# Kernel tuning notes

Measured on AMD Instinct MI355X. Metric: run time of the kernel, lower is better.

The kernel has to match this reference:

```python
import jax, jax.numpy as jnp
import numpy as np

B, T, N, D = 16, 12, 2048, 128  # T*D == 12*hidden_dim, D == hidden_dim (structural constraint)


def _lin(key, out_dim, in_dim):
    k1, k2 = jax.random.split(key)
    s = 1.0 / np.sqrt(in_dim)
    W = jax.random.uniform(k1, (out_dim, in_dim), jnp.float32, -s, s)
    b = jax.random.uniform(k2, (out_dim,), jnp.float32, -s, s)
    return W, b


def setup_inputs() -> dict:
    key = jax.random.key(0)
    ks = jax.random.split(key, 12)
    x = jax.random.normal(ks[0], (B, T, N, D), jnp.float32)
    Wd1, bd1 = _lin(ks[1], D, 12 * D)      # conv_down[0] (1x1 conv == linear over channels)
    Wd2, bd2 = _lin(ks[2], D, D)           # conv_down[3]
    Wq, bq = _lin(ks[3], D, D)
    Wk, bk = _lin(ks[4], D, D)
    Wv, bv = _lin(ks[5], D, D)
    Wu1, bu1 = _lin(ks[6], 12 * D, D)      # conv_up[0]
    Wu2, bu2 = _lin(ks[7], 12 * D, 12 * D) # conv_up[3]
    gamma = jnp.ones((D,), jnp.float32)
    beta = jnp.zeros((D,), jnp.float32)
    Wr1, br1 = _lin(ks[8], D, D)
    Wr2, br2 = _lin(ks[9], D, D)
    Wi1, bi1 = _lin(ks[10], D, D)
    Wi2, bi2 = _lin(ks[11], D, D)
    return dict(x=x, Wd1=Wd1, bd1=bd1, Wd2=Wd2, bd2=bd2, Wq=Wq, bq=bq, Wk=Wk, bk=bk,
                Wv=Wv, bv=bv, Wu1=Wu1, bu1=bu1, Wu2=Wu2, bu2=bu2, gamma=gamma, beta=beta,
                Wr1=Wr1, br1=br1, Wr2=Wr2, br2=br2, Wi1=Wi1, bi1=bi1, Wi2=Wi2, bi2=bi2)


def _mlp(x, W1, b1, W2, b2):
    # Linear -> GELU(exact, torch default) -> (Dropout=identity in eval) -> Linear
    return jax.nn.gelu(x @ W1.T + b1, approximate=False) @ W2.T + b2


def reference(x, Wd1, bd1, Wd2, bd2, Wq, bq, Wk, bk, Wv, bv, Wu1, bu1, Wu2, bu2,
              gamma, beta, Wr1, br1, Wr2, br2, Wi1, bi1, Wi2, bi2):
    Bx, Tx, Nx, d = x.shape
    # ---- node self-attention branch ----
    xt = jnp.transpose(x, (0, 2, 1, 3)).reshape(Bx, Nx, Tx * d)        # [B,N,T*d]
    y = jax.nn.relu(xt @ Wd1.T + bd1) @ Wd2.T + bd2                     # conv_down: [B,N,d]
    q = y @ Wq.T + bq
    k = y @ Wk.T + bk
    v = y @ Wv.T + bv
    scale = 1.0 / jnp.sqrt(jnp.float32(d // 2))                         # dk = hidden_dim // 2
    scores = jax.nn.softmax(jnp.einsum('bnd,bmd->bnm', q, k) * scale, axis=-1)
    o = jnp.einsum('bnm,bmd->bnd', scores, v)                           # [B,N,d]
    o = jax.nn.relu(o @ Wu1.T + bu1) @ Wu2.T + bu2                      # conv_up: [B,N,12d]
    out_node = jnp.transpose(o.reshape(Bx, Nx, Tx, d), (0, 2, 1, 3))    # [B,T,N,d]
    # ---- residual + LayerNorm ----
    h1 = out_node + x
    mu = jnp.mean(h1, axis=-1, keepdims=True)
    var = jnp.mean(jnp.square(h1 - mu), axis=-1, keepdims=True)
    hn = (h1 - mu) / jnp.sqrt(var + 1e-5) * gamma + beta
    # ---- FFT dual-path MLP over time axis ----
    hf = jnp.fft.rfft(hn, axis=1)                                        # [B,T//2+1,N,d] complex
    re, im = jnp.real(hf), jnp.imag(hf)
    hr = _mlp(re, Wr1, br1, Wr2, br2) - _mlp(im, Wi1, bi1, Wi2, bi2)
    hi = _mlp(re, Wi1, bi1, Wi2, bi2) + _mlp(im, Wr1, br1, Wr2, br2)
    hc = jax.lax.complex(hr, hi)
    out = jnp.fft.irfft(hc, n=Tx, axis=1) + x
    return out
```

## Files before the change

### kernel.cpp

```cpp
#include <hip/hip_runtime.h>
#include <math.h>

#define T_ 12
#define N_ 2048
#define D_ 128
#define ND_ 262144
#define TND_ 3145728L

typedef __attribute__((ext_vector_type(8))) short short8;
typedef __attribute__((ext_vector_type(4))) float f32x4;

__device__ __forceinline__ ushort f2b(float f) {
  unsigned u = __float_as_uint(f);
  u += 0x7fffu + ((u >> 16) & 1u);
  return (ushort)(u >> 16);
}
__device__ __forceinline__ float b2f(ushort s) {
  return __uint_as_float(((unsigned)s) << 16);
}

__device__ __forceinline__ void gload16(const ushort* g, ushort* lds) {
  __builtin_amdgcn_global_load_lds(
      (const __attribute__((address_space(1))) void*)g,
      (__attribute__((address_space(3))) void*)lds, 16, 0, 0);
}

__constant__ float COS12[12] = {
    1.0f, 0.8660254037844387f, 0.5f, 0.0f, -0.5f, -0.8660254037844387f,
    -1.0f, -0.8660254037844387f, -0.5f, 0.0f, 0.5f, 0.8660254037844387f};
__constant__ float SIN12[12] = {
    0.0f, 0.5f, 0.8660254037844387f, 1.0f, 0.8660254037844387f, 0.5f,
    0.0f, -0.5f, -0.8660254037844387f, -1.0f, -0.8660254037844387f, -0.5f};

template <int ACT, int OUT>
__global__ __launch_bounds__(256) void mgemm(
    const ushort* __restrict__ A, const ushort* __restrict__ B,
    const float* __restrict__ bias, void* __restrict__ Cv,
    int K, int lda, int ldb, int ldc, float alpha,
    long sAb, long sBb, long sCb, int off0, int off1) {
  __shared__ ushort As[4096];
  __shared__ ushort Bs[4096];
  const int tid = threadIdx.x;
  const int w = tid >> 6;
  const int l = tid & 63;
  const int lr = l & 15;
  const int lg = l >> 4;
  const int row0 = blockIdx.y * 128;
  const int col0 = blockIdx.x * 128;
  const ushort* Ap = A + sAb * blockIdx.z;
  const ushort* Bp = B + sBb * blockIdx.z;

  f32x4 acc[2][8];
#pragma unroll
  for (int i = 0; i < 2; ++i)
#pragma unroll
    for (int j = 0; j < 8; ++j) acc[i][j] = (f32x4){0.f, 0.f, 0.f, 0.f};

  const int ba = w, bb2 = w + 4;
  const ushort* Apl = Ap + (long)(row0 + ba * 16 + lr) * lda + lg * 8;
  const ushort* Apl2 = Ap + (long)(row0 + bb2 * 16 + lr) * lda + lg * 8;
  const ushort* Bpl = Bp + (long)(col0 + ba * 16 + lr) * ldb + lg * 8;
  const ushort* Bpl2 = Bp + (long)(col0 + bb2 * 16 + lr) * ldb + lg * 8;
  for (int k0 = 0; k0 < K; k0 += 32) {
    gload16(Apl + k0, As + ba * 512);
    gload16(Apl2 + k0, As + bb2 * 512);
    gload16(Bpl + k0, Bs + ba * 512);
    gload16(Bpl2 + k0, Bs + bb2 * 512);
    __syncthreads();
    const short8 a0 = *(const short8*)(As + (w * 2 + 0) * 512 + l * 8);
    const short8 a1 = *(const short8*)(As + (w * 2 + 1) * 512 + l * 8);
#pragma unroll
    for (int ni = 0; ni < 8; ++ni) {
      const short8 bfr = *(const short8*)(Bs + ni * 512 + l * 8);
      acc[0][ni] = __builtin_amdgcn_mfma_f32_16x16x32_bf16(a0, bfr, acc[0][ni], 0, 0, 0);
      acc[1][ni] = __builtin_amdgcn_mfma_f32_16x16x32_bf16(a1, bfr, acc[1][ni], 0, 0, 0);
    }
    __syncthreads();
  }

  const long Cz = sCb * blockIdx.z;
#pragma unroll
  for (int mi = 0; mi < 2; ++mi) {
    const int grow0 = row0 + w * 32 + mi * 16 + lg * 4;
    if (OUT == 2) {
      ushort* C = (ushort*)Cv;
#pragma unroll
      for (int ni = 0; ni < 8; ++ni) {
        const int c = col0 + ni * 16 + lr;
        const float bv = bias ? bias[c] : 0.f;
        ushort4 pk;
        float v0 = acc[mi][ni][0] * alpha + bv;
        float v1 = acc[mi][ni][1] * alpha + bv;
        float v2 = acc[mi][ni][2] * alpha + bv;
        float v3 = acc[mi][ni][3] * alpha + bv;
        if (ACT == 1) { v0 = fmaxf(v0, 0.f); v1 = fmaxf(v1, 0.f); v2 = fmaxf(v2, 0.f); v3 = fmaxf(v3, 0.f); }
        pk.x = f2b(v0); pk.y = f2b(v1); pk.z = f2b(v2); pk.w = f2b(v3);
        *(ushort4*)(C + (long)c * ldc + grow0) = pk;
      }
    } else {
#pragma unroll
      for (int ni = 0; ni < 8; ++ni) {
        const int c = col0 + ni * 16 + lr;
        const float bv = bias ? bias[c] : 0.f;
        const int cm = c + (c < 128 ? off0 : off1);
#pragma unroll
        for (int r = 0; r < 4; ++r) {
          float v = acc[mi][ni][r] * alpha + bv;
          if (ACT == 1) v = fmaxf(v, 0.f);
          if (ACT == 2) v = 0.5f * v * (1.0f + erff(v * 0.7071067811865475f));
          const long off = Cz + (long)(grow0 + r) * ldc + cm;
          if (OUT == 0) ((float*)Cv)[off] = v;
          else ((ushort*)Cv)[off] = f2b(v);
        }
      }
    }
  }
}

__global__ __launch_bounds__(256) void mgemm_ln(
    const ushort* __restrict__ A, const ushort* __restrict__ B,
    const float* __restrict__ bias, const float* __restrict__ x,
    const float* __restrict__ gamma, const float* __restrict__ beta,
    float* __restrict__ hn) {
  const int K = 1536;
  __shared__ ushort As[4096];
  __shared__ ushort Bs[4096];
  const int tid = threadIdx.x;
  const int w = tid >> 6;
  const int l = tid & 63;
  const int lr = l & 15;
  const int lg = l >> 4;
  const int row0 = blockIdx.y * 128;
  const int t = blockIdx.x;
  const int col0 = t * 128;

  f32x4 acc[2][8];
#pragma unroll
  for (int i = 0; i < 2; ++i)
#pragma unroll
    for (int j = 0; j < 8; ++j) acc[i][j] = (f32x4){0.f, 0.f, 0.f, 0.f};

  const int ba = w, bb2 = w + 4;
  const ushort* Apl = A + (long)(row0 + ba * 16 + lr) * K + lg * 8;
  const ushort* Apl2 = A + (long)(row0 + bb2 * 16 + lr) * K + lg * 8;
  const ushort* Bpl = B + (long)(col0 + ba * 16 + lr) * K + lg * 8;
  const ushort* Bpl2 = B + (long)(col0 + bb2 * 16 + lr) * K + lg * 8;
  for (int k0 = 0; k0 < K; k0 += 32) {
    gload16(Apl + k0, As + ba * 512);
    gload16(Apl2 + k0, As + bb2 * 512);
    gload16(Bpl + k0, Bs + ba * 512);
    gload16(Bpl2 + k0, Bs + bb2 * 512);
    __syncthreads();
    const short8 a0 = *(const short8*)(As + (w * 2 + 0) * 512 + l * 8);
    const short8 a1 = *(const short8*)(As + (w * 2 + 1) * 512 + l * 8);
#pragma unroll
    for (int ni = 0; ni < 8; ++ni) {
      const short8 bfr = *(const short8*)(Bs + ni * 512 + l * 8);
      acc[0][ni] = __builtin_amdgcn_mfma_f32_16x16x32_bf16(a0, bfr, acc[0][ni], 0, 0, 0);
      acc[1][ni] = __builtin_amdgcn_mfma_f32_16x16x32_bf16(a1, bfr, acc[1][ni], 0, 0, 0);
    }
    __syncthreads();
  }

#pragma unroll
  for (int mi = 0; mi < 2; ++mi) {
#pragma unroll
    for (int r = 0; r < 4; ++r) {
      const int gr = row0 + w * 32 + mi * 16 + lg * 4 + r;
      const int bb = gr >> 11;
      const int nn = gr & 2047;
      const long base = ((long)(bb * 12 + t) << 18) + (long)nn * 128;
      float h[8];
      float s1 = 0.f, s2 = 0.f;
#pragma unroll
      for (int ni = 0; ni < 8; ++ni) {
        const int d = ni * 16 + lr;
        const float v = acc[mi][ni][r] + bias[col0 + d] + x[base + d];
        h[ni] = v;
        s1 += v;
        s2 += v * v;
      }
#pragma unroll
      for (int m = 1; m < 16; m <<= 1) {
        s1 += __shfl_xor(s1, m);
        s2 += __shfl_xor(s2, m);
      }
      const float mu = s1 * (1.f / 128.f);
      const float rstd = rsqrtf(s2 * (1.f / 128.f) - mu * mu + 1e-5f);
#pragma unroll
      for (int ni = 0; ni < 8; ++ni) {
        const int d = ni * 16 + lr;
        hn[base + d] = (h[ni] - mu) * rstd * gamma[d] + beta[d];
      }
    }
  }
}

__global__ __launch_bounds__(256) void softmax_k(const float* __restrict__ S,
                                                 ushort* __restrict__ P) {
  const long row = ((long)blockIdx.y * N_ + blockIdx.x) * N_;
  const float* p = S + row;
  const int tid = threadIdx.x;
  float v[8];
  float mx = -3.4e38f;
#pragma unroll
  for (int j = 0; j < 8; ++j) {
    v[j] = p[tid + 256 * j];
    mx = fmaxf(mx, v[j]);
  }
  __shared__ float red[256];
  red[tid] = mx;
  __syncthreads();
  for (int s = 128; s > 0; s >>= 1) {
    if (tid < s) red[tid] = fmaxf(red[tid], red[tid + s]);
    __syncthreads();
  }
  mx = red[0];
  __syncthreads();
  float sum = 0.0f;
#pragma unroll
  for (int j = 0; j < 8; ++j) {
    v[j] = expf(v[j] - mx);
    sum += v[j];
  }
  red[tid] = sum;
  __syncthreads();
  for (int s = 128; s > 0; s >>= 1) {
    if (tid < s) red[tid] += red[tid + s];
    __syncthreads();
  }
  const float inv = 1.0f / red[0];
#pragma unroll
  for (int j = 0; j < 8; ++j) P[row + tid + 256 * j] = f2b(v[j] * inv);
}

__global__ __launch_bounds__(256) void rfft_k(const float* __restrict__ hn,
                                              ushort* __restrict__ re,
                                              ushort* __restrict__ im) {
  const long i = (long)blockIdx.x * 256 + threadIdx.x;
  const int bb = (int)(i >> 18);
  const int nd = (int)(i & (ND_ - 1));
  float ht[12];
#pragma unroll
  for (int t = 0; t < 12; ++t) ht[t] = hn[((long)(bb * T_ + t) << 18) + nd];
#pragma unroll
  for (int f = 0; f < 7; ++f) {
    float sr = 0.0f, si = 0.0f;
#pragma unroll
    for (int t = 0; t < 12; ++t) {
      const int k = (f * t) % 12;
      sr = fmaf(ht[t], COS12[k], sr);
      si = fmaf(ht[t], SIN12[k], si);
    }
    const long off = ((long)(bb * 7 + f) << 18) + nd;
    re[off] = f2b(sr);
    im[off] = f2b(-si);
  }
}

__global__ __launch_bounds__(256) void irfft_k(const float* __restrict__ hr,
                                               const float* __restrict__ hi,
                                               const float* __restrict__ x,
                                               float* __restrict__ out) {
  const long i = (long)blockIdx.x * 256 + threadIdx.x;
  const int bb = (int)(i >> 18);
  const int nd = (int)(i & (ND_ - 1));
  float r[7], m[7];
#pragma unroll
  for (int f = 0; f < 7; ++f) {
    const long off = ((long)(bb * 7 + f) << 18) + nd;
    r[f] = hr[off];
    m[f] = hi[off];
  }
#pragma unroll
  for (int t = 0; t < 12; ++t) {
    float s = r[0] + ((t & 1) ? -r[6] : r[6]);
#pragma unroll
    for (int f = 1; f < 6; ++f) {
      const int k = (f * t) % 12;
      s += 2.0f * (r[f] * COS12[k] - m[f] * SIN12[k]);
    }
    const long xi = ((long)(bb * T_ + t) << 18) + nd;
    out[xi] = s * (1.0f / 12.0f) + x[xi];
  }
}

__global__ __launch_bounds__(256) void xt_k(const float* __restrict__ x,
                                            ushort* __restrict__ xt) {
  const long i = (long)blockIdx.x * 256 + threadIdx.x;
  const int d = (int)(i & 127);
  const long r = i >> 7;
  const int nn = (int)(r & 2047);
  const long r2 = r >> 11;
  const int t = (int)(r2 % 12);
  const int bb = (int)(r2 / 12);
  xt[((long)bb * 2048 + nn) * 1536 + t * 128 + d] = f2b(x[i]);
}

__global__ __launch_bounds__(256) void prep_k(
    const float* Wd1, const float* Wd2, const float* Wq, const float* Wk,
    const float* Wv, const float* Wu1, const float* Wu2, const float* Wr1,
    const float* Wr2, const float* Wi1, const float* Wi2,
    const float* bq, const float* bk, const float* br1, const float* bi1,
    const float* br2, const float* bi2,
    ushort* __restrict__ wws, float* __restrict__ bws) {
  const long i = (long)blockIdx.x * 256 + threadIdx.x;
  if (i < 256) bws[i] = (i < 128) ? bq[i] : bk[i - 128];
  else if (i < 512) { const int j = i - 256; bws[i] = (j < 128) ? br1[j] : bi1[j - 128]; }
  else if (i < 768) { const int j = i - 512; bws[i] = (j < 128) ? bi1[j] : br1[j - 128]; }
  else if (i < 896) { const int j = i - 768; bws[i] = br2[j] - bi2[j]; }
  else if (i < 1024) { const int j = i - 896; bws[i] = bi2[j] + br2[j]; }
  if (i >= 2949120) return;
  float v;
  if (i < 196608) v = Wd1[i];
  else if (i < 212992) v = Wd2[i - 196608];
  else if (i < 245760) { const long j = i - 212992; v = (j < 16384) ? Wq[j] : Wk[j - 16384]; }
  else if (i < 262144) v = Wv[i - 245760];
  else if (i < 458752) v = Wu1[i - 262144];
  else if (i < 2818048) v = Wu2[i - 458752];
  else if (i < 2850816) { const long j = i - 2818048; v = (j < 16384) ? Wr1[j] : Wi1[j - 16384]; }
  else if (i < 2883584) { const long j = i - 2850816; v = (j < 16384) ? Wi1[j] : Wr1[j - 16384]; }
  else if (i < 2916352) {
    const long j = i - 2883584; const int n = (int)(j >> 8), k = (int)(j & 255);
    v = (k < 128) ? Wr2[n * 128 + k] : -Wi2[n * 128 + k - 128];
  } else {
    const long j = i - 2916352; const int n = (int)(j >> 8), k = (int)(j & 255);
    v = (k < 128) ? Wi2[n * 128 + k] : Wr2[n * 128 + k - 128];
  }
  wws[i] = f2b(v);
}

extern "C" void kernel_launch(void* const* d_in, const int* in_sizes, int n_in,
                              void* d_out, int out_size, void* d_ws,
                              size_t ws_size, hipStream_t stream) {
  (void)in_sizes; (void)n_in; (void)out_size;
  const float* x   = (const float*)d_in[0];
  const float* Wd1 = (const float*)d_in[1];
  const float* bd1 = (const float*)d_in[2];
  const float* Wd2 = (const float*)d_in[3];
  const float* bd2 = (const float*)d_in[4];
  const float* Wq  = (const float*)d_in[5];
  const float* bq  = (const float*)d_in[6];
  const float* Wk  = (const float*)d_in[7];
  const float* bk  = (const float*)d_in[8];
  const float* Wv  = (const float*)d_in[9];
  const float* bv  = (const float*)d_in[10];
  const float* Wu1 = (const float*)d_in[11];
  const float* bu1 = (const float*)d_in[12];
  const float* Wu2 = (const float*)d_in[13];
  const float* bu2 = (const float*)d_in[14];
  const float* gamma = (const float*)d_in[15];
  const float* beta  = (const float*)d_in[16];
  const float* Wr1 = (const float*)d_in[17];
  const float* br1 = (const float*)d_in[18];
  const float* Wr2 = (const float*)d_in[19];
  const float* br2 = (const float*)d_in[20];
  const float* Wi1 = (const float*)d_in[21];
  const float* bi1 = (const float*)d_in[22];
  const float* Wi2 = (const float*)d_in[23];
  const float* bi2 = (const float*)d_in[24];
  float* out = (float*)d_out;

  float* bws = (float*)d_ws;
  ushort* wws = (ushort*)(bws + 1024);
  const size_t kFixed = 1024 * 4 + 2949120 * 2;
  const size_t kPerBatch = 90177536;
  int CB = 1;
  const int cands[5] = {16, 8, 4, 2, 1};
  for (int ci = 0; ci < 5; ++ci)
    if (kFixed + (size_t)cands[ci] * kPerBatch <= ws_size) { CB = cands[ci]; break; }

  char* base = (char*)d_ws + kFixed;
  const long R = (long)CB * N_;
  const long Fr = (long)CB * 7 * N_;
  ushort* xt  = (ushort*)base;
  ushort* y1  = xt  + CB * 3145728L;
  ushort* y   = y1  + R * 128;
  ushort* qkb = y   + R * 128;
  ushort* vT  = qkb + R * 256;
  ushort* P   = vT  + R * 128;
  ushort* o   = P   + (long)CB * N_ * N_;
  ushort* u1  = o   + R * 128;
  ushort* re  = u1  + R * 1536;
  ushort* im  = re  + Fr * 128;
  ushort* G   = im  + Fr * 128;
  float*  S   = (float*)(G + Fr * 512);
  float*  hn  = S   + (long)CB * N_ * N_;
  float*  hr  = hn  + R * 1536;
  float*  hi  = hr  + Fr * 128;

  const dim3 blk(256);
  const float scale = 0.125f;

  prep_k<<<dim3(11520), blk, 0, stream>>>(Wd1, Wd2, Wq, Wk, Wv, Wu1, Wu2,
                                          Wr1, Wr2, Wi1, Wi2, bq, bk, br1,
                                          bi1, br2, bi2, wws, bws);
  ushort* Wd1b = wws;
  ushort* Wd2b = wws + 196608;
  ushort* Wqkb = wws + 212992;
  ushort* Wvb  = wws + 245760;
  ushort* Wu1b = wws + 262144;
  ushort* Wu2b = wws + 458752;
  ushort* W13b = wws + 2818048;
  ushort* W24b = wws + 2850816;
  ushort* Whrb = wws + 2883584;
  ushort* Whib = wws + 2916352;
  float* bqk = bws;
  float* b13 = bws + 256;
  float* b24 = bws + 512;
  float* bhr = bws + 768;
  float* bhi = bws + 896;

  for (int c = 0; c < 16 / CB; ++c) {
    const int b0 = c * CB;
    const float* xc = x + (long)b0 * TND_;
    float* oc = out + (long)b0 * TND_;
    const int GY = CB * 16;
    const int GF = CB * 112;

    xt_k<<<dim3(CB * 12288), blk, 0, stream>>>(xc, xt);
    mgemm<1, 1><<<dim3(1, GY), blk, 0, stream>>>(
        xt, Wd1b, bd1, y1, 1536, 1536, 1536, 128, 1.f, 0, 0, 0, 0, 0);
    mgemm<0, 1><<<dim3(1, GY), blk, 0, stream>>>(
        y1, Wd2b, bd2, y, 128, 128, 128, 128, 1.f, 0, 0, 0, 0, 0);
    mgemm<0, 1><<<dim3(2, GY), blk, 0, stream>>>(
        y, Wqkb, bqk, qkb, 128, 128, 128, 256, 1.f, 0, 0, 0, 0, 0);
    mgemm<0, 2><<<dim3(1, GY), blk, 0, stream>>>(
        y, Wvb, bv, vT, 128, 128, 128, (int)R, 1.f, 0, 0, 0, 0, 0);
    mgemm<0, 0><<<dim3(16, 16, CB), blk, 0, stream>>>(
        qkb, qkb + 128, nullptr, S, 128, 256, 256, 2048, scale,
        524288, 524288, 4194304, 0, 0);
    softmax_k<<<dim3(N_, CB), blk, 0, stream>>>(S, P);
    mgemm<0, 1><<<dim3(1, 16, CB), blk, 0, stream>>>(
        P, vT, nullptr, o, 2048, 2048, (int)R, 128, 1.f,
        4194304, 2048, 262144, 0, 0);
    mgemm<1, 1><<<dim3(12, GY), blk, 0, stream>>>(
        o, Wu1b, bu1, u1, 128, 128, 128, 1536, 1.f, 0, 0, 0, 0, 0);
    mgemm_ln<<<dim3(12, GY), blk, 0, stream>>>(u1, Wu2b, bu2, xc, gamma, beta, hn);
    rfft_k<<<dim3(CB * 1024), blk, 0, stream>>>(hn, re, im);
    mgemm<2, 1><<<dim3(2, GF), blk, 0, stream>>>(
        re, W13b, b13, G, 128, 128, 128, 512, 1.f, 0, 0, 0, 0, 128);
    mgemm<2, 1><<<dim3(2, GF), blk, 0, stream>>>(
        im, W24b, b24, G, 128, 128, 128, 512, 1.f, 0, 0, 0, 128, 256);
    mgemm<0, 0><<<dim3(1, GF), blk, 0, stream>>>(
        G, Whrb, bhr, hr, 256, 512, 256, 128, 1.f, 0, 0, 0, 0, 0);
    mgemm<0, 0><<<dim3(1, GF), blk, 0, stream>>>(
        G + 256, Whib, bhi, hi, 256, 512, 256, 128, 1.f, 0, 0, 0, 0, 0);
    irfft_k<<<dim3(CB * 1024), blk, 0, stream>>>(hr, hi, xc, oc);
  }
}
```

Before: 1.823 ms.

## Fuse FFT dual-path MLP GEMMs into one register-resident kernel

Replaces four GEMM launches for the frequency-domain MLPs (two first-layer GEMMs writing the GELU intermediate G to global memory, then two second-layer GEMMs reading it back) with a single kernel. Each wave computes both first-layer products for its 32 rows, applies GELU, and packs the results to bf16 in registers. It then rearranges them into MFMA A-fragments with lane shuffles and runs the second-layer GEMM directly. This removes the global round-trip of the intermediate and three launches. In exchange it loads weights straight from global without LDS staging, recomputes the first layer once per output half, and raises register pressure.

```diff
diff --git a/kernel.cpp b/kernel.cpp
--- a/kernel.cpp
+++ b/kernel.cpp
@@ -9,6 +9,7 @@
 
 typedef __attribute__((ext_vector_type(8))) short short8;
 typedef __attribute__((ext_vector_type(4))) float f32x4;
+typedef __attribute__((ext_vector_type(4))) unsigned int u32x4;
 
 __device__ __forceinline__ ushort f2b(float f) {
   unsigned u = __float_as_uint(f);
@@ -18,6 +19,11 @@
 __device__ __forceinline__ float b2f(ushort s) {
   return __uint_as_float(((unsigned)s) << 16);
 }
+__device__ __forceinline__ float gelu_f(float v) {
+  return 0.5f * v * (1.0f + erff(v * 0.7071067811865475f));
+}
+
+typedef union { short8 s8; u32x4 u; } frag_u;
 
 __device__ __forceinline__ void gload16(const ushort* g, ushort* lds) {
   __builtin_amdgcn_global_load_lds(
@@ -192,6 +198,129 @@
         const int d = ni * 16 + lr;
         hn[base + d] = (h[ni] - mu) * rstd * gamma[d] + beta[d];
       }
+    }
+  }
+}
+
+__global__ __launch_bounds__(256) void fft_mlp_k(
+    const ushort* __restrict__ re, const ushort* __restrict__ im,
+    const ushort* __restrict__ Wr1, const ushort* __restrict__ Wi1,
+    const float* __restrict__ br1, const float* __restrict__ bi1,
+    const ushort* __restrict__ Whr, const ushort* __restrict__ Whi,
+    const float* __restrict__ bhr, const float* __restrict__ bhi,
+    float* __restrict__ hr, float* __restrict__ hi) {
+  const int tid = threadIdx.x;
+  const int w = tid >> 6;
+  const int l = tid & 63;
+  const int lr = l & 15;
+  const int lg = l >> 4;
+  const long m0 = (long)blockIdx.x * 128 + w * 32;
+  const int srcA = lr + ((lg & 1) << 5);
+  const int srcB = srcA + 16;
+  const bool top = (lg >= 2);
+
+  for (int h = 0; h < 2; ++h) {
+    const ushort* W1e = h ? Wi1 : Wr1;
+    const float*  b1e = h ? bi1 : br1;
+    const ushort* W1o = h ? Wr1 : Wi1;
+    const float*  b1o = h ? br1 : bi1;
+    const ushort* W2  = h ? Whi : Whr;
+    const float*  b2  = h ? bhi : bhr;
+    float* outp = h ? hi : hr;
+
+    unsigned p0[2][8][2], p1[2][8][2];
+#pragma unroll
+    for (int gi = 0; gi < 2; ++gi) {
+      const ushort* Asrc = gi ? im : re;
+      const ushort* W1 = gi ? W1o : W1e;
+      const float* b1 = gi ? b1o : b1e;
+      f32x4 acc[2][8];
+#pragma unroll
+      for (int i = 0; i < 2; ++i)
+#pragma unroll
+        for (int j = 0; j < 8; ++j) acc[i][j] = (f32x4){0.f, 0.f, 0.f, 0.f};
+#pragma unroll
+      for (int kc = 0; kc < 4; ++kc) {
+        frag_u bf0, bf1;
+        bf0.u = *(const u32x4*)(Asrc + (m0 + lr) * 128 + kc * 32 + lg * 8);
+        bf1.u = *(const u32x4*)(Asrc + (m0 + 16 + lr) * 128 + kc * 32 + lg * 8);
+#pragma unroll
+        for (int ni = 0; ni < 8; ++ni) {
+          frag_u af;
+          af.u = *(const u32x4*)(W1 + (ni * 16 + lr) * 128 + kc * 32 + lg * 8);
+          acc[0][ni] = __builtin_amdgcn_mfma_f32_16x16x32_bf16(af.s8, bf0.s8, acc[0][ni], 0, 0, 0);
+          acc[1][ni] = __builtin_amdgcn_mfma_f32_16x16x32_bf16(af.s8, bf1.s8, acc[1][ni], 0, 0, 0);
+        }
+      }
+#pragma unroll
+      for (int ni = 0; ni < 8; ++ni) {
+        float bb0 = b1[ni * 16 + lg * 4 + 0];
+        float bb1 = b1[ni * 16 + lg * 4 + 1];
+        float bb2 = b1[ni * 16 + lg * 4 + 2];
+        float bb3 = b1[ni * 16 + lg * 4 + 3];
+#pragma unroll
+        for (int mi = 0; mi < 2; ++mi) {
+          float v0 = gelu_f(acc[mi][ni][0] + bb0);
+          float v1 = gelu_f(acc[mi][ni][1] + bb1);
+          float v2 = gelu_f(acc[mi][ni][2] + bb2);
+          float v3 = gelu_f(acc[mi][ni][3] + bb3);
+          unsigned w0 = (unsigned)f2b(v0) | ((unsigned)f2b(v1) << 16);
+          unsigned w1 = (unsigned)f2b(v2) | ((unsigned)f2b(v3) << 16);
+          if (gi == 0) { p0[mi][ni][0] = w0; p0[mi][ni][1] = w1; }
+          else         { p1[mi][ni][0] = w0; p1[mi][ni][1] = w1; }
+        }
+      }
+    }
+
+    f32x4 acc2[2][8];
+#pragma unroll
+    for (int i = 0; i < 2; ++i)
+#pragma unroll
+      for (int j = 0; j < 8; ++j) acc2[i][j] = (f32x4){0.f, 0.f, 0.f, 0.f};
+#pragma unroll
+    for (int c = 0; c < 8; ++c) {
+      const int cp = c & 3;
+      frag_u A0, A1;
+#pragma unroll
+      for (int mi = 0; mi < 2; ++mi) {
+        unsigned q00, q01, q10, q11;
+        if (c < 4) {
+          q00 = p0[mi][2 * cp][0];     q01 = p0[mi][2 * cp][1];
+          q10 = p0[mi][2 * cp + 1][0]; q11 = p0[mi][2 * cp + 1][1];
+        } else {
+          q00 = p1[mi][2 * cp][0];     q01 = p1[mi][2 * cp][1];
+          q10 = p1[mi][2 * cp + 1][0]; q11 = p1[mi][2 * cp + 1][1];
+        }
+        unsigned lo0 = (unsigned)__shfl((int)q00, srcA);
+        unsigned lo1 = (unsigned)__shfl((int)q01, srcA);
+        unsigned lo2 = (unsigned)__shfl((int)q00, srcB);
+        unsigned lo3 = (unsigned)__shfl((int)q01, srcB);
+        unsigned h0 = (unsigned)__shfl((int)q10, srcA);
+        unsigned h1 = (unsigned)__shfl((int)q11, srcA);
+        unsigned h2 = (unsigned)__shfl((int)q10, srcB);
+        unsigned h3 = (unsigned)__shfl((int)q11, srcB);
+        frag_u& A = mi ? A1 : A0;
+        A.u[0] = top ? h0 : lo0;
+        A.u[1] = top ? h1 : lo1;
+        A.u[2] = top ? h2 : lo2;
+        A.u[3] = top ? h3 : lo3;
+      }
+#pragma unroll
+      for (int ni = 0; ni < 8; ++ni) {
+        frag_u bf;
+        bf.u = *(const u32x4*)(W2 + (ni * 16 + lr) * 256 + c * 32 + lg * 8);
+        acc2[0][ni] = __builtin_amdgcn_mfma_f32_16x16x32_bf16(A0.s8, bf.s8, acc2[0][ni], 0, 0, 0);
+        acc2[1][ni] = __builtin_amdgcn_mfma_f32_16x16x32_bf16(A1.s8, bf.s8, acc2[1][ni], 0, 0, 0);
+      }
+    }
+#pragma unroll
+    for (int ni = 0; ni < 8; ++ni) {
+      const float bb = b2[ni * 16 + lr];
+#pragma unroll
+      for (int mi = 0; mi < 2; ++mi)
+#pragma unroll
+        for (int r = 0; r < 4; ++r)
+          outp[(m0 + mi * 16 + lg * 4 + r) * 128 + ni * 16 + lr] = acc2[mi][ni][r] + bb;
     }
   }
 }
@@ -402,12 +531,9 @@
   ushort* Wu1b = wws + 262144;
   ushort* Wu2b = wws + 458752;
   ushort* W13b = wws + 2818048;
-  ushort* W24b = wws + 2850816;
   ushort* Whrb = wws + 2883584;
   ushort* Whib = wws + 2916352;
   float* bqk = bws;
-  float* b13 = bws + 256;
-  float* b24 = bws + 512;
   float* bhr = bws + 768;
   float* bhi = bws + 896;
 
@@ -438,14 +564,8 @@
         o, Wu1b, bu1, u1, 128, 128, 128, 1536, 1.f, 0, 0, 0, 0, 0);
     mgemm_ln<<<dim3(12, GY), blk, 0, stream>>>(u1, Wu2b, bu2, xc, gamma, beta, hn);
     rfft_k<<<dim3(CB * 1024), blk, 0, stream>>>(hn, re, im);
-    mgemm<2, 1><<<dim3(2, GF), blk, 0, stream>>>(
-        re, W13b, b13, G, 128, 128, 128, 512, 1.f, 0, 0, 0, 0, 128);
-    mgemm<2, 1><<<dim3(2, GF), blk, 0, stream>>>(
-        im, W24b, b24, G, 128, 128, 128, 512, 1.f, 0, 0, 0, 128, 256);
-    mgemm<0, 0><<<dim3(1, GF), blk, 0, stream>>>(
-        G, Whrb, bhr, hr, 256, 512, 256, 128, 1.f, 0, 0, 0, 0, 0);
-    mgemm<0, 0><<<dim3(1, GF), blk, 0, stream>>>(
-        G + 256, Whib, bhi, hi, 256, 512, 256, 128, 1.f, 0, 0, 0, 0, 0);
+    fft_mlp_k<<<dim3(GF), blk, 0, stream>>>(
+        re, im, W13b, W13b + 16384, br1, bi1, Whrb, Whib, bhr, bhi, hr, hi);
     irfft_k<<<dim3(CB * 1024), blk, 0, stream>>>(hr, hi, xc, oc);
   }
 }
```

Result: slower. 2.130 ms (+16.8%).
